# Kernel optimization log

Measured on AMD Instinct MI355X. Metric: run time of the kernel, lower is better.

## Reference

```python
import jax, jax.numpy as jnp
import numpy as np

N_NODES = 100000
N_EDGES = 625000
DIM = 128

def setup_inputs() -> dict:
    key = jax.random.key(0)
    k1, k2, k3, k4 = jax.random.split(key, 4)
    scale = 1.0 / np.sqrt(DIM)
    x = jax.random.normal(k1, (N_NODES, DIM), dtype=jnp.float32)
    edge_index = jax.random.randint(k2, (2, N_EDGES), 0, N_NODES, dtype=jnp.int64)
    W_l = jax.random.normal(k3, (DIM, DIM), dtype=jnp.float32) * scale
    W_r = jax.random.normal(k4, (DIM, DIM), dtype=jnp.float32) * scale
    b = jnp.zeros((DIM,), dtype=jnp.float32)
    return {"x": x, "edge_index": edge_index, "W_l": W_l, "W_r": W_r, "b": b}

def reference(x, edge_index, W_l, W_r, b):
    # PyG SAGEConv (mean aggr): out_i = W_l @ mean_{j in N(i)} x_j + W_r @ x_i + b
    n = x.shape[0]
    src = edge_index[0]  # message sources
    dst = edge_index[1]  # message targets
    msgs = x[src]                                             # [E, D] gather
    agg = jax.ops.segment_sum(msgs, dst, num_segments=n)      # [N, D] scatter-add
    cnt = jax.ops.segment_sum(jnp.ones((src.shape[0],), dtype=x.dtype), dst, num_segments=n)
    mean = agg / jnp.maximum(cnt, 1.0)[:, None]               # mean aggregation
    out = mean @ W_l.T + x @ W_r.T + b                        # neighbor + root transform
    out = jax.nn.relu(out)
    # dropout in eval mode = identity; original returns (x, edge_attr=None)
    return out
```

## Files before the change

### kernel.cpp

```cpp
#include <hip/hip_runtime.h>

#define NNODES 100000
#define NEDGES 625000
#define DIM 128
#define NTILES 782
#define ZBLK 98
#define BCAP 64

typedef short short8 __attribute__((ext_vector_type(8)));
typedef unsigned short ushort8 __attribute__((ext_vector_type(8)));
typedef float f32x4  __attribute__((ext_vector_type(4)));

__device__ __forceinline__ unsigned short f2bf(float f) {
    unsigned u = __float_as_uint(f);
    u += 0x7FFFu + ((u >> 16) & 1u);
    return (unsigned short)(u >> 16);
}
__device__ __forceinline__ float bf_lo(unsigned u) { return __uint_as_float(u << 16); }
__device__ __forceinline__ float bf_hi(unsigned u) { return __uint_as_float(u & 0xFFFF0000u); }

template<bool ZBF>
__global__ __launch_bounds__(512, 4) void gemm_zero_kernel(
    const float* __restrict__ x,
    const float* __restrict__ Wl,
    const float* __restrict__ Wr,
    unsigned short* __restrict__ Yh,
    unsigned short* __restrict__ Zh,
    float* __restrict__ Z,
    int* __restrict__ cnt)
{
    __shared__ unsigned short wfrag[32768];
    const int tid = threadIdx.x;

    if (blockIdx.x >= NTILES) {
        int i = (blockIdx.x - NTILES) * 1024 + tid * 2;
        if (i < NNODES) {
            if (i + 1 < NNODES) *(int2*)(cnt + i) = (int2){0, 0};
            else cnt[i] = 0;
        }
        return;
    }

    const int wave = tid >> 6;
    const int lane = tid & 63;
    const int lrow = lane & 15;
    const int kgrp = lane >> 4;
    const int row0 = blockIdx.x * 128 + wave * 16;

#pragma unroll
    for (int it = 0; it < 8; ++it) {
        const int i  = it * 512 + tid;
        const int il = i & 63;
        const int ks = (i >> 6) & 3;
        const int ct = i >> 8;
        const int r  = ct * 16 + (il & 15);
        const int k8 = ks * 4 + (il >> 4);
        const float* wr = ((r < DIM) ? (Wl + (size_t)r * DIM)
                                     : (Wr + (size_t)(r - DIM) * DIM)) + k8 * 8;
        float4 w0 = *(const float4*)(wr);
        float4 w1 = *(const float4*)(wr + 4);
        ushort8 c;
        c[0] = f2bf(w0.x); c[1] = f2bf(w0.y); c[2] = f2bf(w0.z); c[3] = f2bf(w0.w);
        c[4] = f2bf(w1.x); c[5] = f2bf(w1.y); c[6] = f2bf(w1.z); c[7] = f2bf(w1.w);
        *(ushort8*)(wfrag + (size_t)i * 8) = c;
    }
    __syncthreads();

    int arow = row0 + lrow;
    if (arow >= NNODES) arow = NNODES - 1;
    const float* xrow = x + (size_t)arow * DIM + kgrp * 8;

    f32x4 acc[16];
#pragma unroll
    for (int i = 0; i < 16; ++i) acc[i] = (f32x4){0.f, 0.f, 0.f, 0.f};

#pragma unroll
    for (int ks = 0; ks < 4; ++ks) {
        float4 a0 = *(const float4*)(xrow + ks * 32);
        float4 a1 = *(const float4*)(xrow + ks * 32 + 4);
        short8 af;
        af[0] = (short)f2bf(a0.x); af[1] = (short)f2bf(a0.y);
        af[2] = (short)f2bf(a0.z); af[3] = (short)f2bf(a0.w);
        af[4] = (short)f2bf(a1.x); af[5] = (short)f2bf(a1.y);
        af[6] = (short)f2bf(a1.z); af[7] = (short)f2bf(a1.w);
#pragma unroll
        for (int ct = 0; ct < 16; ++ct) {
            short8 bf = *(const short8*)(wfrag + (size_t)((ct * 4 + ks) * 64 + lane) * 8);
            acc[ct] = __builtin_amdgcn_mfma_f32_16x16x32_bf16(af, bf, acc[ct], 0, 0, 0);
        }
    }

#pragma unroll
    for (int r = 0; r < 4; ++r) {
        const int row = row0 + kgrp * 4 + r;
        if (row < NNODES) {
            ushort8 y;
#pragma unroll
            for (int ct = 0; ct < 8; ++ct) y[ct] = f2bf(acc[ct][r]);
            *(ushort8*)(Yh + (size_t)row * DIM + lrow * 8) = y;
            if (ZBF) {
                ushort8 zz;
#pragma unroll
                for (int ct = 0; ct < 8; ++ct) zz[ct] = f2bf(acc[ct + 8][r]);
                *(ushort8*)(Zh + (size_t)row * DIM + lrow * 8) = zz;
            } else {
                float4 z0, z1;
                z0.x = acc[8][r];  z0.y = acc[9][r];  z0.z = acc[10][r]; z0.w = acc[11][r];
                z1.x = acc[12][r]; z1.y = acc[13][r]; z1.z = acc[14][r]; z1.w = acc[15][r];
                *(float4*)(Z + (size_t)row * DIM + lrow * 8)     = z0;
                *(float4*)(Z + (size_t)row * DIM + lrow * 8 + 4) = z1;
            }
        }
    }
}

__global__ void fill_kernel(const int* __restrict__ ei,
                            int* __restrict__ cnt, int* __restrict__ adjb) {
    int e = blockIdx.x * 256 + threadIdx.x;
    if (e >= NEDGES) return;
    int src = ei[e];
    int dst = ei[NEDGES + e];
    int p = atomicAdd(&cnt[dst], 1);
    if (p < BCAP) adjb[(size_t)dst * BCAP + p] = src;
}

template<bool ZBF>
__global__ __launch_bounds__(256) void aggregate_kernel(
    const unsigned short* __restrict__ Yh,
    const unsigned short* __restrict__ Zh,
    const int* __restrict__ cnt,
    const int* __restrict__ adjb,
    const float* __restrict__ bias,
    float* __restrict__ out)
{
    const int tid = threadIdx.x;
    const int l16 = tid & 15;
    const int n = blockIdx.x * 16 + (tid >> 4);
    if (n >= NNODES) return;

    int deg = cnt[n];
    if (deg > BCAP) deg = BCAP;

    float bb[8], z[8];
#pragma unroll
    for (int m = 0; m < 8; ++m) bb[m] = bias[16 * m + l16];
    if (ZBF) {
        uint4 zv = *(const uint4*)(Zh + (size_t)n * DIM + l16 * 8);
        z[0] = bf_lo(zv.x); z[1] = bf_hi(zv.x); z[2] = bf_lo(zv.y); z[3] = bf_hi(zv.y);
        z[4] = bf_lo(zv.z); z[5] = bf_hi(zv.z); z[6] = bf_lo(zv.w); z[7] = bf_hi(zv.w);
    } else {
        float4 z0 = *(const float4*)(out + (size_t)n * DIM + l16 * 8);
        float4 z1 = *(const float4*)(out + (size_t)n * DIM + l16 * 8 + 4);
        z[0] = z0.x; z[1] = z0.y; z[2] = z0.z; z[3] = z0.w;
        z[4] = z1.x; z[5] = z1.y; z[6] = z1.z; z[7] = z1.w;
    }

    float a[8];
#pragma unroll
    for (int m = 0; m < 8; ++m) a[m] = 0.f;

    const int* bkt = adjb + (size_t)n * BCAP;
    for (int j = 0; j < deg; j += 8) {
        const int rem = deg - j;
        int s[8];
#pragma unroll
        for (int k = 0; k < 8; ++k) {
            int idx = j + k;
            s[k] = bkt[(idx < deg) ? idx : (deg - 1)];
        }
        uint4 v[8];
#pragma unroll
        for (int k = 0; k < 8; ++k)
            v[k] = *(const uint4*)(Yh + (size_t)s[k] * DIM + l16 * 8);
#pragma unroll
        for (int k = 0; k < 8; ++k) {
            if (k < rem) {
                a[0] += bf_lo(v[k].x); a[1] += bf_hi(v[k].x);
                a[2] += bf_lo(v[k].y); a[3] += bf_hi(v[k].y);
                a[4] += bf_lo(v[k].z); a[5] += bf_hi(v[k].z);
                a[6] += bf_lo(v[k].w); a[7] += bf_hi(v[k].w);
            }
        }
    }

    const float invd = 1.0f / fmaxf((float)deg, 1.0f);
#pragma unroll
    for (int m = 0; m < 8; ++m)
        out[(size_t)n * DIM + 16 * m + l16] = fmaxf(a[m] * invd + z[m] + bb[m], 0.f);
}

extern "C" void kernel_launch(void* const* d_in, const int* in_sizes, int n_in,
                              void* d_out, int out_size, void* d_ws, size_t ws_size,
                              hipStream_t stream) {
    const float* x  = (const float*)d_in[0];
    const int*   ei = (const int*)d_in[1];
    const float* Wl = (const float*)d_in[2];
    const float* Wr = (const float*)d_in[3];
    const float* b  = (const float*)d_in[4];
    float* out = (float*)d_out;

    int*            cnt  = (int*)d_ws;
    int*            adjb = (int*)((char*)d_ws + (1ull << 20));
    unsigned short* Yh   = (unsigned short*)((char*)d_ws + (27ull << 20));
    unsigned short* Zh   = (unsigned short*)((char*)d_ws + (53ull << 20));

    const size_t need_zbf = (53ull << 20) + (size_t)NNODES * DIM * 2;
    const bool zbf = (ws_size >= need_zbf);

    if (zbf) {
        gemm_zero_kernel<true><<<NTILES + ZBLK, 512, 0, stream>>>(x, Wl, Wr, Yh, Zh, out, cnt);
        fill_kernel<<<(NEDGES + 255) / 256, 256, 0, stream>>>(ei, cnt, adjb);
        aggregate_kernel<true><<<(NNODES + 15) / 16, 256, 0, stream>>>(Yh, Zh, cnt, adjb, b, out);
    } else {
        gemm_zero_kernel<false><<<NTILES + ZBLK, 512, 0, stream>>>(x, Wl, Wr, Yh, Zh, out, cnt);
        fill_kernel<<<(NEDGES + 255) / 256, 256, 0, stream>>>(ei, cnt, adjb);
        aggregate_kernel<false><<<(NNODES + 15) / 16, 256, 0, stream>>>(Yh, Zh, cnt, adjb, b, out);
    }
}
```

Before: 99.37 us.

## Split GEMM into two half-weight passes to halve LDS and raise occupancy

The fused GEMM kernel now stages only one weight matrix (W_l, then W_r) in a 32 KB shared buffer instead of both in 64 KB, running two passes with 8 accumulators each. It also loads and converts the x tile to bf16 once up front and keeps it in registers, so the global loads overlap the weight staging. The launch-bounds occupancy hint goes from 4 to 6 blocks per CU, with less LDS and fewer live accumulators. In exchange it adds extra barriers and a second weight-staging phase per block, which serialise work inside each block.

```diff
diff --git a/kernel.cpp b/kernel.cpp
--- a/kernel.cpp
+++ b/kernel.cpp
@@ -20,7 +20,7 @@
 __device__ __forceinline__ float bf_hi(unsigned u) { return __uint_as_float(u & 0xFFFF0000u); }
 
 template<bool ZBF>
-__global__ __launch_bounds__(512, 4) void gemm_zero_kernel(
+__global__ __launch_bounds__(512, 6) void gemm_zero_kernel(
     const float* __restrict__ x,
     const float* __restrict__ Wl,
     const float* __restrict__ Wr,
@@ -29,7 +29,7 @@
     float* __restrict__ Z,
     int* __restrict__ cnt)
 {
-    __shared__ unsigned short wfrag[32768];
+    __shared__ unsigned short wfrag[16384];
     const int tid = threadIdx.x;
 
     if (blockIdx.x >= NTILES) {
@@ -47,16 +47,28 @@
     const int kgrp = lane >> 4;
     const int row0 = blockIdx.x * 128 + wave * 16;
 
-#pragma unroll
-    for (int it = 0; it < 8; ++it) {
+    int arow = row0 + lrow;
+    if (arow >= NNODES) arow = NNODES - 1;
+    const float* xrow = x + (size_t)arow * DIM + kgrp * 8;
+    short8 af[4];
+#pragma unroll
+    for (int ks = 0; ks < 4; ++ks) {
+        float4 a0 = *(const float4*)(xrow + ks * 32);
+        float4 a1 = *(const float4*)(xrow + ks * 32 + 4);
+        af[ks][0] = (short)f2bf(a0.x); af[ks][1] = (short)f2bf(a0.y);
+        af[ks][2] = (short)f2bf(a0.z); af[ks][3] = (short)f2bf(a0.w);
+        af[ks][4] = (short)f2bf(a1.x); af[ks][5] = (short)f2bf(a1.y);
+        af[ks][6] = (short)f2bf(a1.z); af[ks][7] = (short)f2bf(a1.w);
+    }
+
+#pragma unroll
+    for (int it = 0; it < 4; ++it) {
         const int i  = it * 512 + tid;
         const int il = i & 63;
         const int ks = (i >> 6) & 3;
         const int ct = i >> 8;
-        const int r  = ct * 16 + (il & 15);
-        const int k8 = ks * 4 + (il >> 4);
-        const float* wr = ((r < DIM) ? (Wl + (size_t)r * DIM)
-                                     : (Wr + (size_t)(r - DIM) * DIM)) + k8 * 8;
+        const float* wr = Wl + (size_t)(ct * 16 + (il & 15)) * DIM
+                             + (ks * 4 + (il >> 4)) * 8;
         float4 w0 = *(const float4*)(wr);
         float4 w1 = *(const float4*)(wr + 4);
         ushort8 c;
@@ -66,49 +78,75 @@
     }
     __syncthreads();
 
-    int arow = row0 + lrow;
-    if (arow >= NNODES) arow = NNODES - 1;
-    const float* xrow = x + (size_t)arow * DIM + kgrp * 8;
-
-    f32x4 acc[16];
-#pragma unroll
-    for (int i = 0; i < 16; ++i) acc[i] = (f32x4){0.f, 0.f, 0.f, 0.f};
-
-#pragma unroll
-    for (int ks = 0; ks < 4; ++ks) {
-        float4 a0 = *(const float4*)(xrow + ks * 32);
-        float4 a1 = *(const float4*)(xrow + ks * 32 + 4);
-        short8 af;
-        af[0] = (short)f2bf(a0.x); af[1] = (short)f2bf(a0.y);
-        af[2] = (short)f2bf(a0.z); af[3] = (short)f2bf(a0.w);
-        af[4] = (short)f2bf(a1.x); af[5] = (short)f2bf(a1.y);
-        af[6] = (short)f2bf(a1.z); af[7] = (short)f2bf(a1.w);
-#pragma unroll
-        for (int ct = 0; ct < 16; ++ct) {
-            short8 bf = *(const short8*)(wfrag + (size_t)((ct * 4 + ks) * 64 + lane) * 8);
-            acc[ct] = __builtin_amdgcn_mfma_f32_16x16x32_bf16(af, bf, acc[ct], 0, 0, 0);
-        }
-    }
-
-#pragma unroll
-    for (int r = 0; r < 4; ++r) {
-        const int row = row0 + kgrp * 4 + r;
-        if (row < NNODES) {
-            ushort8 y;
-#pragma unroll
-            for (int ct = 0; ct < 8; ++ct) y[ct] = f2bf(acc[ct][r]);
-            *(ushort8*)(Yh + (size_t)row * DIM + lrow * 8) = y;
-            if (ZBF) {
-                ushort8 zz;
-#pragma unroll
-                for (int ct = 0; ct < 8; ++ct) zz[ct] = f2bf(acc[ct + 8][r]);
-                *(ushort8*)(Zh + (size_t)row * DIM + lrow * 8) = zz;
-            } else {
-                float4 z0, z1;
-                z0.x = acc[8][r];  z0.y = acc[9][r];  z0.z = acc[10][r]; z0.w = acc[11][r];
-                z1.x = acc[12][r]; z1.y = acc[13][r]; z1.z = acc[14][r]; z1.w = acc[15][r];
-                *(float4*)(Z + (size_t)row * DIM + lrow * 8)     = z0;
-                *(float4*)(Z + (size_t)row * DIM + lrow * 8 + 4) = z1;
+    {
+        f32x4 acc[8];
+#pragma unroll
+        for (int i = 0; i < 8; ++i) acc[i] = (f32x4){0.f, 0.f, 0.f, 0.f};
+#pragma unroll
+        for (int ks = 0; ks < 4; ++ks)
+#pragma unroll
+            for (int ct = 0; ct < 8; ++ct) {
+                short8 bf = *(const short8*)(wfrag + (size_t)((ct * 4 + ks) * 64 + lane) * 8);
+                acc[ct] = __builtin_amdgcn_mfma_f32_16x16x32_bf16(af[ks], bf, acc[ct], 0, 0, 0);
+            }
+#pragma unroll
+        for (int r = 0; r < 4; ++r) {
+            const int row = row0 + kgrp * 4 + r;
+            if (row < NNODES) {
+                ushort8 y;
+#pragma unroll
+                for (int ct = 0; ct < 8; ++ct) y[ct] = f2bf(acc[ct][r]);
+                *(ushort8*)(Yh + (size_t)row * DIM + lrow * 8) = y;
+            }
+        }
+    }
+
+    __syncthreads();
+
+#pragma unroll
+    for (int it = 0; it < 4; ++it) {
+        const int i  = it * 512 + tid;
+        const int il = i & 63;
+        const int ks = (i >> 6) & 3;
+        const int ct = i >> 8;
+        const float* wr = Wr + (size_t)(ct * 16 + (il & 15)) * DIM
+                             + (ks * 4 + (il >> 4)) * 8;
+        float4 w0 = *(const float4*)(wr);
+        float4 w1 = *(const float4*)(wr + 4);
+        ushort8 c;
+        c[0] = f2bf(w0.x); c[1] = f2bf(w0.y); c[2] = f2bf(w0.z); c[3] = f2bf(w0.w);
+        c[4] = f2bf(w1.x); c[5] = f2bf(w1.y); c[6] = f2bf(w1.z); c[7] = f2bf(w1.w);
+        *(ushort8*)(wfrag + (size_t)i * 8) = c;
+    }
+    __syncthreads();
+
+    {
+        f32x4 acc[8];
+#pragma unroll
+        for (int i = 0; i < 8; ++i) acc[i] = (f32x4){0.f, 0.f, 0.f, 0.f};
+#pragma unroll
+        for (int ks = 0; ks < 4; ++ks)
+#pragma unroll
+            for (int ct = 0; ct < 8; ++ct) {
+                short8 bf = *(const short8*)(wfrag + (size_t)((ct * 4 + ks) * 64 + lane) * 8);
+                acc[ct] = __builtin_amdgcn_mfma_f32_16x16x32_bf16(af[ks], bf, acc[ct], 0, 0, 0);
+            }
+#pragma unroll
+        for (int r = 0; r < 4; ++r) {
+            const int row = row0 + kgrp * 4 + r;
+            if (row < NNODES) {
+                if (ZBF) {
+                    ushort8 zz;
+#pragma unroll
+                    for (int ct = 0; ct < 8; ++ct) zz[ct] = f2bf(acc[ct][r]);
+                    *(ushort8*)(Zh + (size_t)row * DIM + lrow * 8) = zz;
+                } else {
+                    float4 z0, z1;
+                    z0.x = acc[0][r]; z0.y = acc[1][r]; z0.z = acc[2][r]; z0.w = acc[3][r];
+                    z1.x = acc[4][r]; z1.y = acc[5][r]; z1.z = acc[6][r]; z1.w = acc[7][r];
+                    *(float4*)(Z + (size_t)row * DIM + lrow * 8)     = z0;
+                    *(float4*)(Z + (size_t)row * DIM + lrow * 8 + 4) = z1;
+                }
             }
         }
     }
```

After: 100.1 us. About the same (+0.8%).
